# Performance work log

Measured on AMD Instinct MI355X. Metric: run time of the kernel, lower is better.

The kernel has to match this reference:

```python
import jax, jax.numpy as jnp
import numpy as np

B, T, S = 32, 64, 64
V, E, H, Hs = 32000, 512, 512, 512
D2 = 2 * Hs  # src feature dim


def setup_inputs() -> dict:
    key = jax.random.key(0)
    ks = jax.random.split(key, 26)
    n = lambda k, shape, s=0.05: (jax.random.normal(k, shape, jnp.float32) * s)
    inp = {
        'src': jax.random.normal(ks[0], (B, S, D2), jnp.float32),
        'trg': jax.random.randint(ks[1], (B, T), 0, V),
        'mask': jnp.ones((B, T), jnp.float32),
        'emb': n(ks[2], (V, E)),
        # PyTorch LSTMCell params: weight_ih [4H, E+H], weight_hh [4H, H]
        'f_Wih': n(ks[3], (4 * H, E + H)), 'f_Whh': n(ks[4], (4 * H, H)),
        'f_bih': n(ks[5], (4 * H,)), 'f_bhh': n(ks[6], (4 * H,)),
        'b_Wih': n(ks[7], (4 * H, E + H)), 'b_Whh': n(ks[8], (4 * H, H)),
        'b_bih': n(ks[9], (4 * H,)), 'b_bhh': n(ks[10], (4 * H,)),
        # attention projections: hidden -> 2*src_hidden
        'fatt_W': n(ks[11], (D2, H)), 'fatt_b': n(ks[12], (D2,)),
        'batt_W': n(ks[13], (D2, H)), 'batt_b': n(ks[14], (D2,)),
        # att_hidden linears: (H + 2*Hs) -> H
        'fah_W': n(ks[15], (H, H + D2)), 'fah_b': n(ks[16], (H,)),
        'bah_W': n(ks[17], (H, H + D2)), 'bah_b': n(ks[18], (H,)),
        # output projection 2H -> V
        'fc_W': n(ks[19], (V, 2 * H)), 'fc_b': n(ks[20], (V,)),
        'feed_init': n(ks[21], (2 * H,), 1.0),
        'hid_init': n(ks[22], (4 * H,), 1.0),
    }
    return inp


def reference(src, trg, mask, emb, f_Wih, f_Whh, f_bih, f_bhh,
              b_Wih, b_Whh, b_bih, b_bhh, fatt_W, fatt_b, batt_W, batt_b,
              fah_W, fah_b, bah_W, bah_b, fc_W, fc_b, feed_init, hid_init):
    Bn = src.shape[0]
    Hn = feed_init.shape[0] // 2
    scale = 1.0 / np.sqrt(Hn)  # key.size(-1) == trg hidden before projection

    x = emb[trg]  # [B, T, E]  (dropout p=0 -> identity)

    hhat0 = jnp.broadcast_to(feed_init, (Bn, 2 * Hn))
    f_hhat0, b_hhat0 = jnp.split(hhat0, 2, axis=1)
    hid0 = jnp.broadcast_to(hid_init, (Bn, 4 * Hn))
    f_hid, b_hid = jnp.split(hid0, 2, axis=-1)
    f_h0, f_c0 = jnp.split(f_hid, 2, axis=-1)
    b_h0, b_c0 = jnp.split(b_hid, 2, axis=-1)

    def lstm(xin, h, c, Wih, Whh, bih, bhh):
        g = xin @ Wih.T + bih + h @ Whh.T + bhh
        i, f, gg, o = jnp.split(g, 4, axis=-1)
        c = jax.nn.sigmoid(f) * c + jax.nn.sigmoid(i) * jnp.tanh(gg)
        h = jax.nn.sigmoid(o) * jnp.tanh(c)
        return h, c

    def att(h, W, b):
        k = h @ W.T + b                              # [B, 2Hs]
        w = jnp.einsum('bd,bsd->bs', k, src) * scale  # [B, S]
        p = jax.nn.softmax(w, axis=-1)
        return jnp.einsum('bs,bsd->bd', p, src)       # [B, 2Hs]

    xs = jnp.swapaxes(x, 0, 1)      # [T, B, E]
    ms = jnp.swapaxes(mask, 0, 1)   # [T, B]

    def f_step(carry, x_t):
        h, c, hhat = carry
        h, c = lstm(jnp.concatenate([x_t, hhat], -1), h, c, f_Wih, f_Whh, f_bih, f_bhh)
        ct = att(h, fatt_W, fatt_b)
        # NOTE: original uses b_att_hidden in the forward loop (faithful)
        hhat = jnp.tanh(jnp.concatenate([h, ct], -1) @ bah_W.T + bah_b)
        return (h, c, hhat), hhat

    _, f_out = jax.lax.scan(f_step, (f_h0, f_c0, f_hhat0), xs)  # [T, B, H]

    def b_step(carry, inp):
        x_t, m_t = inp
        h, c, hhat = carry
        hn, cn = lstm(jnp.concatenate([x_t, hhat], -1), h, c, b_Wih, b_Whh, b_bih, b_bhh)
        h = m_t[:, None] * hn
        c = m_t[:, None] * cn
        ct = att(h, batt_W, batt_b)
        # NOTE: original uses f_att_hidden in the backward loop (faithful)
        hhat = jnp.tanh(jnp.concatenate([h, ct], -1) @ fah_W.T + fah_b)
        return (h, c, hhat), hhat

    _, b_out = jax.lax.scan(b_step, (b_h0, b_c0, b_hhat0), (xs[::-1], ms[::-1]))

    f_out = jnp.swapaxes(f_out, 0, 1)        # [B, T, H]
    b_cheat = jnp.swapaxes(b_out, 0, 1)      # reversed-time order, as stacked in torch
    # b_outputs[:, :-2] = b_outputs_cheat[:, 2:]; last two steps zero (faithful)
    b_shift = jnp.concatenate([b_cheat[:, 2:], jnp.zeros_like(b_cheat[:, :2])], axis=1)

    logits = jnp.concatenate([f_out, b_shift], -1) @ fc_W.T + fc_b  # [B, T, V]
    return logits
```

## Files before the change

### kernel.cpp

```cpp
#include <hip/hip_runtime.h>
#include <hip/hip_bf16.h>
#include <math.h>

typedef __hip_bfloat16 bf16;
typedef __attribute__((ext_vector_type(8))) short short8b;
typedef __attribute__((ext_vector_type(8))) __bf16 bf16x8;
typedef __attribute__((ext_vector_type(4))) float f32x4;

#define SCALE_F 0.04419417382415922f

template <typename V>
static __device__ inline auto mfma_try(V a, V b, f32x4 c, int)
    -> decltype(__builtin_amdgcn_mfma_f32_16x16x32_bf16(a, b, c, 0, 0, 0)) {
  return __builtin_amdgcn_mfma_f32_16x16x32_bf16(a, b, c, 0, 0, 0);
}
template <typename V>
static __device__ inline auto mfma_try(V a, V b, f32x4 c, long)
    -> decltype(__builtin_amdgcn_mfma_f32_16x16x32_bf16(
        __builtin_bit_cast(bf16x8, a), __builtin_bit_cast(bf16x8, b), c, 0, 0, 0)) {
  return __builtin_amdgcn_mfma_f32_16x16x32_bf16(
      __builtin_bit_cast(bf16x8, a), __builtin_bit_cast(bf16x8, b), c, 0, 0, 0);
}
static __device__ inline f32x4 MFMA(short8b a, short8b b, f32x4 c) {
  return mfma_try(a, b, c, 0);
}

static __device__ inline short8b ldb8(const bf16* p) {
  return *reinterpret_cast<const short8b*>(p);
}
static __device__ inline float b2f(bf16 v) { return __bfloat162float(v); }
static __device__ inline bf16 f2b(float v) { return __float2bfloat16(v); }
static __device__ inline float s2f(short s) {
  unsigned u = ((unsigned)(unsigned short)s) << 16;
  return __builtin_bit_cast(float, u);
}
static __device__ inline unsigned pack2(float lo, float hi) {
  const unsigned a = (unsigned)__builtin_bit_cast(unsigned short, f2b(lo));
  const unsigned b = (unsigned)__builtin_bit_cast(unsigned short, f2b(hi));
  return a | (b << 16);
}
static __device__ inline float sigm(float x) { return 1.f / (1.f + expf(-x)); }

static __device__ inline void st2_wt(bf16* p, float v) {
  unsigned ud = (unsigned)__builtin_bit_cast(unsigned short, f2b(v));
  asm volatile("global_store_short %0, %1, off sc0 sc1" ::"v"(p), "v"(ud)
               : "memory");
}
static __device__ inline void st4_wt(bf16* p, float lo, float hi) {
  unsigned ud = pack2(lo, hi);
  asm volatile("global_store_dword %0, %1, off sc0 sc1" ::"v"(p), "v"(ud)
               : "memory");
}

static __device__ inline void st_flag(unsigned* p, unsigned v) {
  asm volatile("global_store_dword %0, %1, off sc0 sc1" ::"v"(p), "v"(v)
               : "memory");
}
static __device__ inline unsigned ld_flag(const unsigned* p) {
  unsigned v;
  asm volatile("global_load_dword %0, %1, off sc0 sc1\n\ts_waitcnt vmcnt(0)"
               : "=v"(v)
               : "v"(p)
               : "memory");
  return v;
}

static __device__ inline void gbar(unsigned* flags, unsigned ep, int blk, int tid) {
  asm volatile("s_waitcnt vmcnt(0)" ::: "memory");
  __syncthreads();
  if (tid < 64) {
    unsigned* row = flags + (size_t)ep * 64;
    if (tid == 0) st_flag(row + blk, 1u);
    while (true) {
      const unsigned v = ld_flag(row + tid);
      if (__ballot(v != 0) == ~0ull) break;
      __builtin_amdgcn_s_sleep(1);
    }
  }
  __syncthreads();
}

template <typename OutT, bool HAS_BIAS>
__global__ __launch_bounds__(256) void gemm_k(
    const bf16* __restrict__ A, const bf16* __restrict__ Bw,
    OutT* __restrict__ C, const float* __restrict__ bias,
    int M, int N, int K) {
  const int lane = threadIdx.x & 63;
  const int wid = threadIdx.x >> 6;
  const int m0 = blockIdx.y * 128 + (wid >> 1) * 64;
  const int n0 = blockIdx.x * 128 + (wid & 1) * 64;
  const int lr = lane & 15;
  const int lk = (lane >> 4) * 8;
  f32x4 acc[4][4];
#pragma unroll
  for (int i = 0; i < 4; ++i)
#pragma unroll
    for (int j = 0; j < 4; ++j) acc[i][j] = (f32x4){0.f, 0.f, 0.f, 0.f};
  const bf16* Ap = A + (size_t)(m0 + lr) * K + lk;
  const bf16* Bp = Bw + (size_t)(n0 + lr) * K + lk;
  for (int k0 = 0; k0 < K; k0 += 32) {
    short8b av[4], bv[4];
#pragma unroll
    for (int i = 0; i < 4; ++i) av[i] = ldb8(Ap + (size_t)i * 16 * K + k0);
#pragma unroll
    for (int i = 0; i < 4; ++i) bv[i] = ldb8(Bp + (size_t)i * 16 * K + k0);
#pragma unroll
    for (int mi = 0; mi < 4; ++mi)
#pragma unroll
      for (int ni = 0; ni < 4; ++ni)
        acc[mi][ni] = MFMA(av[mi], bv[ni], acc[mi][ni]);
  }
  const int rb = (lane >> 4) * 4;
#pragma unroll
  for (int mi = 0; mi < 4; ++mi) {
#pragma unroll
    for (int r = 0; r < 4; ++r) {
      const int row = m0 + mi * 16 + rb + r;
#pragma unroll
      for (int ni = 0; ni < 4; ++ni) {
        const int col = n0 + ni * 16 + lr;
        float v = acc[mi][ni][r];
        if (HAS_BIAS) v += bias[col];
        if constexpr (sizeof(OutT) == 2) {
          C[(size_t)row * N + col] = f2b(v);
        } else {
          C[(size_t)row * N + col] = v;
        }
      }
    }
  }
}

__global__ void k_xg(const float* __restrict__ emb, const int* __restrict__ trg,
                     bf16* __restrict__ xg) {
  const int i = blockIdx.x * 256 + threadIdx.x;
  const int r = i >> 9, e = i & 511;
  const int t = r >> 5, b = r & 31;
  const int tok = trg[b * 64 + t];
  xg[i] = f2b(emb[(size_t)tok * 512 + e]);
}

__global__ void k_srcb(const float* __restrict__ s, bf16* __restrict__ d) {
  const int i = blockIdx.x * 256 + threadIdx.x;
  d[i] = f2b(s[i]);
}

__global__ void k_fcw(const float* __restrict__ s, bf16* __restrict__ d) {
  const size_t stride = (size_t)gridDim.x * blockDim.x;
  for (size_t i = blockIdx.x * (size_t)blockDim.x + threadIdx.x;
       i < (size_t)32000 * 1024; i += stride)
    d[i] = f2b(s[i]);
}

__global__ void k_bmt(const bf16* __restrict__ in, bf16* __restrict__ out) {
  const int i = blockIdx.x * 256 + threadIdx.x;
  const int b = i >> 15, rem = i & 32767, o = rem >> 6, s = rem & 63;
  out[i] = in[(size_t)(b * 64 + s) * 512 + o];
}

__global__ void k_wpack(const float* __restrict__ fWih, const float* __restrict__ fWhh,
                        const float* __restrict__ bWih, const float* __restrict__ bWhh,
                        const float* __restrict__ fattW, const float* __restrict__ battW,
                        const float* __restrict__ bahW, const float* __restrict__ fahW,
                        bf16* Wxf, bf16* Wxb, bf16* Wrecf, bf16* Wrecb,
                        bf16* attWtf, bf16* attWtb, bf16* ahW2f, bf16* ahW2b,
                        bf16* Wh1f, bf16* Wh1b) {
  const int stride = gridDim.x * blockDim.x;
  const int i0 = blockIdx.x * blockDim.x + threadIdx.x;
  for (int i = i0; i < 2048 * 512; i += stride) {
    const int gc = i >> 9, k = i & 511;
    Wxf[i] = f2b(fWih[(size_t)gc * 1024 + k]);
    Wxb[i] = f2b(bWih[(size_t)gc * 1024 + k]);
  }
  for (int i = i0; i < 2048 * 1024; i += stride) {
    const int gc = i >> 10, k = i & 1023;
    float vf, vb;
    if (k < 512) { vf = fWih[(size_t)gc * 1024 + 512 + k]; vb = bWih[(size_t)gc * 1024 + 512 + k]; }
    else         { vf = fWhh[(size_t)gc * 512 + k - 512]; vb = bWhh[(size_t)gc * 512 + k - 512]; }
    Wrecf[i] = f2b(vf); Wrecb[i] = f2b(vb);
  }
  for (int i = i0; i < 512 * 1024; i += stride) {
    const int j = i >> 10, d = i & 1023;
    attWtf[i] = f2b(fattW[(size_t)d * 512 + j]);
    attWtb[i] = f2b(battW[(size_t)d * 512 + j]);
  }
  for (int i = i0; i < 512 * 1024; i += stride) {
    const int o = i >> 10, d = i & 1023;
    ahW2f[i] = f2b(bahW[(size_t)o * 1536 + 512 + d]);
    ahW2b[i] = f2b(fahW[(size_t)o * 1536 + 512 + d]);
  }
  for (int i = i0; i < 512 * 512; i += stride) {
    const int o = i >> 9, k = i & 511;
    Wh1f[i] = f2b(bahW[(size_t)o * 1536 + k]);
    Wh1b[i] = f2b(fahW[(size_t)o * 1536 + k]);
  }
}

__global__ void k_c0(const float* __restrict__ src, const float* __restrict__ fb,
                     const float* __restrict__ bb, float* __restrict__ c0f,
                     float* __restrict__ c0b) {
  const int r = blockIdx.x;
  const int tid = threadIdx.x;
  float pf = 0.f, pb = 0.f;
  for (int d = tid; d < 1024; d += 256) {
    const float s = src[(size_t)r * 1024 + d];
    pf += s * fb[d];
    pb += s * bb[d];
  }
#pragma unroll
  for (int d = 1; d < 64; d <<= 1) { pf += __shfl_xor(pf, d); pb += __shfl_xor(pb, d); }
  __shared__ float rf[4], rb2[4];
  if ((tid & 63) == 0) { rf[tid >> 6] = pf; rb2[tid >> 6] = pb; }
  __syncthreads();
  if (tid == 0) {
    c0f[r] = (rf[0] + rf[1] + rf[2] + rf[3]) * SCALE_F;
    c0b[r] = (rb2[0] + rb2[1] + rb2[2] + rb2[3]) * SCALE_F;
  }
}

__global__ void k_init(const float* __restrict__ feed, const float* __restrict__ hid,
                       bf16* hh0, bf16* hh1, bf16* hb0, bf16* hb1,
                       float* cst0, float* cst1) {
  const int i = blockIdx.x * 256 + threadIdx.x;
  const int b = i >> 9, k = i & 511;
  hh0[i] = f2b(feed[k]);
  hh1[i] = f2b(feed[512 + k]);
  hb0[i] = f2b(hid[k]);
  hb1[i] = f2b(hid[1024 + k]);
  cst0[k * 32 + b] = hid[512 + k];
  cst1[k * 32 + b] = hid[1536 + k];
}

struct ScanP {
  const bf16* Wrec[2]; const bf16* Xp[2]; const bf16* Af[2]; const bf16* Bmt[2];
  const bf16* Wh1[2]; const float* bih[2]; const float* bhh[2];
  const float* c0[2]; const float* ahb[2]; const float* mask;
  bf16* hh[2]; bf16* hb[2]; bf16* U[2]; float* cst[2]; bf16* hcat; unsigned* flags;
};

__global__ __launch_bounds__(256) void scan_k(ScanP P) {
  const int blk = blockIdx.x;
  const int dir = blk >> 5;
  const int g = blk & 31;
  const int tid = threadIdx.x;
  const int lane = tid & 63;
  const int wv = tid >> 6;

  const bf16* __restrict__ Wrec = P.Wrec[dir];
  const bf16* __restrict__ Xp = P.Xp[dir];
  const bf16* __restrict__ Af = P.Af[dir];
  const bf16* __restrict__ Bmt = P.Bmt[dir];
  const bf16* __restrict__ Wh1 = P.Wh1[dir];
  const float* __restrict__ bihp = P.bih[dir];
  const float* __restrict__ bhhp = P.bhh[dir];
  const float* __restrict__ c0v = P.c0[dir];
  const float* __restrict__ ahbp = P.ahb[dir];
  bf16* __restrict__ hhB = P.hh[dir];
  bf16* __restrict__ hbB = P.hb[dir];
  bf16* __restrict__ Ubuf = P.U[dir];
  float* __restrict__ cst = P.cst[dir];

  __shared__ float gl[4][16][33];
  __shared__ float h_lds[512];
  __shared__ float w_part[2][64];
  __shared__ float p_lds[64];

  unsigned ep = 0;
  const int lr16 = lane & 15;
  const int kb = lane >> 4;
  const int koff = kb * 8;

  short8b pA0[16], pA1[16];
  {
    const bf16* A0 = hbB + (size_t)lr16 * 512;
    const bf16* A1 = hbB + (size_t)(lr16 + 16) * 512;
#pragma unroll
    for (int ks = 0; ks < 16; ++ks) {
      pA0[ks] = ldb8(A0 + ks * 32 + koff);
      pA1[ks] = ldb8(A1 + ks * 32 + koff);
    }
  }

  for (int t = 0; t < 64; ++t) {
    const bf16* hhR = hhB + (size_t)t * 32 * 512;
    bf16* hhW = hhB + (size_t)(t + 1) * 32 * 512;
    bf16* hbW = hbB + (size_t)(t + 1) * 32 * 512;

    {
      const int gate = wv;
      const int gc = gate * 512 + g * 16 + lr16;
      const bf16* Brow = Wrec + (size_t)gc * 1024;
      const bf16* A0h = hhR + (size_t)lr16 * 512;
      const bf16* A1h = hhR + (size_t)(lr16 + 16) * 512;
      f32x4 ac0 = (f32x4){0.f, 0.f, 0.f, 0.f};
      f32x4 ac1 = (f32x4){0.f, 0.f, 0.f, 0.f};
#pragma unroll
      for (int ks = 0; ks < 16; ++ks) {
        const int k = ks * 32 + koff;
        const short8b bv = ldb8(Brow + 512 + k);
        ac0 = MFMA(pA0[ks], bv, ac0);
        ac1 = MFMA(pA1[ks], bv, ac1);
      }
#pragma unroll
      for (int c = 0; c < 2; ++c) {
        short8b sa[8], sb[8];
#pragma unroll
        for (int i = 0; i < 8; ++i) {
          const int k = (c * 8 + i) * 32 + koff;
          sa[i] = ldb8(A0h + k);
          sb[i] = ldb8(A1h + k);
        }
#pragma unroll
        for (int i = 0; i < 8; ++i) {
          const int k = (c * 8 + i) * 32 + koff;
          const short8b bv = ldb8(Brow + k);
          ac0 = MFMA(sa[i], bv, ac0);
          ac1 = MFMA(sb[i], bv, ac1);
        }
      }
      const int tcol = dir ? (63 - t) : t;
      const float bsum = bihp[gc] + bhhp[gc];
      const bf16* xpc = Xp + (size_t)gc * 2048 + tcol * 32;
#pragma unroll
      for (int r = 0; r < 4; ++r) {
        const int brow = kb * 4 + r;
        gl[gate][lr16][brow] = ac0[r] + b2f(xpc[brow]) + bsum;
        gl[gate][lr16][brow + 16] = ac1[r] + b2f(xpc[brow + 16]) + bsum;
      }
    }
    __syncthreads();
    {
      const int b = tid & 31;
      const int jp = (tid >> 5) * 2;
      float hn2[2];
#pragma unroll
      for (int u = 0; u < 2; ++u) {
        const int jl = jp + u;
        const int j = g * 16 + jl;
        const float gi = gl[0][jl][b];
        const float gf = gl[1][jl][b];
        const float gg = gl[2][jl][b];
        const float go = gl[3][jl][b];
        float cn = sigm(gf) * cst[j * 32 + b] + sigm(gi) * tanhf(gg);
        float hn = sigm(go) * tanhf(cn);
        if (dir) {
          const float m = P.mask[b * 64 + (63 - t)];
          hn *= m; cn *= m;
        }
        cst[j * 32 + b] = cn;
        hn2[u] = hn;
      }
      st4_wt(hbW + (size_t)b * 512 + g * 16 + jp, hn2[0], hn2[1]);
    }
    gbar(P.flags, ep++, blk, tid);

    if (wv == 0) {
      const bf16* Brow = Wh1 + (size_t)(g * 16 + lr16) * 512;
      const bf16* A0 = hbW + (size_t)lr16 * 512;
      const bf16* A1 = hbW + (size_t)(lr16 + 16) * 512;
      f32x4 u0 = (f32x4){0.f, 0.f, 0.f, 0.f};
      f32x4 u1 = (f32x4){0.f, 0.f, 0.f, 0.f};
#pragma unroll
      for (int ks = 0; ks < 16; ++ks) {
        const int k = ks * 32 + koff;
        const short8b bv = ldb8(Brow + k);
        u0 = MFMA(ldb8(A0 + k), bv, u0);
        u1 = MFMA(ldb8(A1 + k), bv, u1);
      }
      bf16* Uw = Ubuf + (size_t)t * 32 * 512;
      const int o = g * 16 + lr16;
#pragma unroll
      for (int r = 0; r < 4; ++r) {
        const int b0 = kb * 4 + r;
        st2_wt(Uw + (size_t)b0 * 512 + o, u0[r]);
        st2_wt(Uw + (size_t)(b0 + 16) * 512 + o, u1[r]);
      }
    } else if (wv == 1) {
      const short8b v = ldb8(hbW + (size_t)g * 512 + lane * 8);
#pragma unroll
      for (int e = 0; e < 8; ++e) h_lds[lane * 8 + e] = s2f(v[e]);
    }
    __syncthreads();
    if (wv == 1 || wv == 2) {
      const int q = wv - 1;
      const bf16* arow = Af + (size_t)(g * 64 + lane) * 512 + q * 256;
      float part = 0.f;
#pragma unroll 8
      for (int k8 = 0; k8 < 256; k8 += 8) {
        const short8b v = ldb8(arow + k8);
#pragma unroll
        for (int e = 0; e < 8; ++e) part += h_lds[q * 256 + k8 + e] * s2f(v[e]);
      }
      w_part[q][lane] = part;
    }
    __syncthreads();
    if (wv == 3) {
      const float v = (w_part[0][lane] + w_part[1][lane]) * SCALE_F + c0v[g * 64 + lane];
      float mx = v;
#pragma unroll
      for (int d = 1; d < 64; d <<= 1) mx = fmaxf(mx, __shfl_xor(mx, d));
      const float e = expf(v - mx);
      float sm = e;
#pragma unroll
      for (int d = 1; d < 64; d <<= 1) sm += __shfl_xor(sm, d);
      p_lds[lane] = e / sm;
    }
    __syncthreads();
    float a2[2];
    {
      const int o2 = tid * 2;
      const bf16* bm0 = Bmt + ((size_t)g * 512 + o2) * 64;
      short8b v0[8], v1[8];
#pragma unroll
      for (int i = 0; i < 8; ++i) {
        v0[i] = ldb8(bm0 + i * 8);
        v1[i] = ldb8(bm0 + 64 + i * 8);
      }
      float s0 = ahbp[o2], s1 = ahbp[o2 + 1];
#pragma unroll
      for (int i = 0; i < 8; ++i)
#pragma unroll
        for (int e = 0; e < 8; ++e) {
          const float p = p_lds[i * 8 + e];
          s0 += p * s2f(v0[i][e]);
          s1 += p * s2f(v1[i][e]);
        }
      a2[0] = s0; a2[1] = s1;
    }
    gbar(P.flags, ep++, blk, tid);

    {
      const int o2 = tid * 2;
      const unsigned uu =
          *reinterpret_cast<const unsigned*>(Ubuf + ((size_t)t * 32 + g) * 512 + o2);
      const float h0 = tanhf(a2[0] + s2f((short)(uu & 0xffffu)));
      const float h1 = tanhf(a2[1] + s2f((short)(uu >> 16)));
      st4_wt(hhW + (size_t)g * 512 + o2, h0, h1);
      const unsigned hp = pack2(h0, h1);
      if (dir == 0) {
        *reinterpret_cast<unsigned*>(P.hcat + (size_t)(g * 64 + t) * 1024 + o2) = hp;
      } else if (t >= 2) {
        *reinterpret_cast<unsigned*>(P.hcat + (size_t)(g * 64 + t - 2) * 1024 + 512 + o2) = hp;
      }
      if (t < 63) {
        const bf16* A0 = hbW + (size_t)lr16 * 512;
        const bf16* A1 = hbW + (size_t)(lr16 + 16) * 512;
#pragma unroll
        for (int ks = 0; ks < 16; ++ks) {
          pA0[ks] = ldb8(A0 + ks * 32 + koff);
          pA1[ks] = ldb8(A1 + ks * 32 + koff);
        }
      }
    }
    gbar(P.flags, ep++, blk, tid);
  }
}

extern "C" void kernel_launch(void* const* d_in, const int* in_sizes, int n_in,
                              void* d_out, int out_size, void* d_ws, size_t ws_size,
                              hipStream_t stream) {
  (void)in_sizes; (void)n_in; (void)out_size; (void)ws_size;
  const float* src  = (const float*)d_in[0];
  const int*   trg  = (const int*)d_in[1];
  const float* mask = (const float*)d_in[2];
  const float* emb  = (const float*)d_in[3];
  const float* fWih = (const float*)d_in[4];
  const float* fWhh = (const float*)d_in[5];
  const float* fbih = (const float*)d_in[6];
  const float* fbhh = (const float*)d_in[7];
  const float* bWih = (const float*)d_in[8];
  const float* bWhh = (const float*)d_in[9];
  const float* bbih = (const float*)d_in[10];
  const float* bbhh = (const float*)d_in[11];
  const float* fattW = (const float*)d_in[12];
  const float* fattb = (const float*)d_in[13];
  const float* battW = (const float*)d_in[14];
  const float* battb = (const float*)d_in[15];
  const float* fahW = (const float*)d_in[16];
  const float* fahb = (const float*)d_in[17];
  const float* bahW = (const float*)d_in[18];
  const float* bahb = (const float*)d_in[19];
  const float* fcW  = (const float*)d_in[20];
  const float* fcb  = (const float*)d_in[21];
  const float* feed = (const float*)d_in[22];
  const float* hid  = (const float*)d_in[23];

  char* wsp = (char*)d_ws;
  size_t off = 0;
  auto alloc = [&](size_t bytes) -> void* {
    void* p = wsp + off;
    off += (bytes + 255) & ~(size_t)255;
    return p;
  };
  unsigned* flags = (unsigned*)alloc((size_t)192 * 64 * 4);
  bf16* hcat = (bf16*)alloc((size_t)2048 * 1024 * 2);
  const size_t zero_bytes = off;
  bf16* xg    = (bf16*)alloc((size_t)2048 * 512 * 2);
  bf16* srcb  = (bf16*)alloc((size_t)2048 * 1024 * 2);
  bf16* fcWb  = (bf16*)alloc((size_t)32000 * 1024 * 2);
  bf16* Wxf   = (bf16*)alloc((size_t)2048 * 512 * 2);
  bf16* Wxb   = (bf16*)alloc((size_t)2048 * 512 * 2);
  bf16* Wrecf = (bf16*)alloc((size_t)2048 * 1024 * 2);
  bf16* Wrecb = (bf16*)alloc((size_t)2048 * 1024 * 2);
  bf16* attWtf = (bf16*)alloc((size_t)512 * 1024 * 2);
  bf16* attWtb = (bf16*)alloc((size_t)512 * 1024 * 2);
  bf16* ahW2f = (bf16*)alloc((size_t)512 * 1024 * 2);
  bf16* ahW2b = (bf16*)alloc((size_t)512 * 1024 * 2);
  bf16* Wh1f  = (bf16*)alloc((size_t)512 * 512 * 2);
  bf16* Wh1b  = (bf16*)alloc((size_t)512 * 512 * 2);
  bf16* Xpf   = (bf16*)alloc((size_t)2048 * 2048 * 2);
  bf16* Xpb   = (bf16*)alloc((size_t)2048 * 2048 * 2);
  bf16* Aff   = (bf16*)alloc((size_t)2048 * 512 * 2);
  bf16* Afb   = (bf16*)alloc((size_t)2048 * 512 * 2);
  bf16* Bmf   = (bf16*)alloc((size_t)2048 * 512 * 2);
  bf16* Bmb   = (bf16*)alloc((size_t)2048 * 512 * 2);
  bf16* Bmtf  = (bf16*)alloc((size_t)2048 * 512 * 2);
  bf16* Bmtb  = (bf16*)alloc((size_t)2048 * 512 * 2);
  float* c0f  = (float*)alloc(2048 * 4);
  float* c0b  = (float*)alloc(2048 * 4);
  bf16* hh0   = (bf16*)alloc((size_t)65 * 32 * 512 * 2);
  bf16* hh1   = (bf16*)alloc((size_t)65 * 32 * 512 * 2);
  bf16* hb0   = (bf16*)alloc((size_t)65 * 32 * 512 * 2);
  bf16* hb1   = (bf16*)alloc((size_t)65 * 32 * 512 * 2);
  bf16* Uf    = (bf16*)alloc((size_t)64 * 32 * 512 * 2);
  bf16* Ub    = (bf16*)alloc((size_t)64 * 32 * 512 * 2);
  float* cst0 = (float*)alloc((size_t)512 * 32 * 4);
  float* cst1 = (float*)alloc((size_t)512 * 32 * 4);

  hipMemsetAsync(d_ws, 0, zero_bytes, stream);

  k_xg<<<4096, 256, 0, stream>>>(emb, trg, xg);
  k_srcb<<<8192, 256, 0, stream>>>(src, srcb);
  k_fcw<<<8192, 256, 0, stream>>>(fcW, fcWb);
  k_wpack<<<2048, 256, 0, stream>>>(fWih, fWhh, bWih, bWhh, fattW, battW, bahW, fahW,
                                    Wxf, Wxb, Wrecf, Wrecb, attWtf, attWtb, ahW2f, ahW2b,
                                    Wh1f, Wh1b);
  k_c0<<<2048, 256, 0, stream>>>(src, fattb, battb, c0f, c0b);
  k_init<<<64, 256, 0, stream>>>(feed, hid, hh0, hh1, hb0, hb1, cst0, cst1);

  gemm_k<bf16, false><<<dim3(16, 16), 256, 0, stream>>>(Wxf, xg, Xpf, nullptr, 2048, 2048, 512);
  gemm_k<bf16, false><<<dim3(16, 16), 256, 0, stream>>>(Wxb, xg, Xpb, nullptr, 2048, 2048, 512);
  gemm_k<bf16, false><<<dim3(4, 16), 256, 0, stream>>>(srcb, attWtf, Aff, nullptr, 2048, 512, 1024);
  gemm_k<bf16, false><<<dim3(4, 16), 256, 0, stream>>>(srcb, attWtb, Afb, nullptr, 2048, 512, 1024);
  gemm_k<bf16, false><<<dim3(4, 16), 256, 0, stream>>>(srcb, ahW2f, Bmf, nullptr, 2048, 512, 1024);
  gemm_k<bf16, false><<<dim3(4, 16), 256, 0, stream>>>(srcb, ahW2b, Bmb, nullptr, 2048, 512, 1024);
  k_bmt<<<4096, 256, 0, stream>>>(Bmf, Bmtf);
  k_bmt<<<4096, 256, 0, stream>>>(Bmb, Bmtb);

  ScanP sp;
  sp.Wrec[0] = Wrecf; sp.Wrec[1] = Wrecb;
  sp.Xp[0] = Xpf;     sp.Xp[1] = Xpb;
  sp.Af[0] = Aff;     sp.Af[1] = Afb;
  sp.Bmt[0] = Bmtf;   sp.Bmt[1] = Bmtb;
  sp.Wh1[0] = Wh1f;   sp.Wh1[1] = Wh1b;
  sp.bih[0] = fbih;   sp.bih[1] = bbih;
  sp.bhh[0] = fbhh;   sp.bhh[1] = bbhh;
  sp.c0[0] = c0f;     sp.c0[1] = c0b;
  sp.ahb[0] = bahb;   sp.ahb[1] = fahb;
  sp.mask = mask;
  sp.hh[0] = hh0;     sp.hh[1] = hh1;
  sp.hb[0] = hb0;     sp.hb[1] = hb1;
  sp.U[0] = Uf;       sp.U[1] = Ub;
  sp.cst[0] = cst0;   sp.cst[1] = cst1;
  sp.hcat = hcat;     sp.flags = flags;
  scan_k<<<64, 256, 0, stream>>>(sp);

  gemm_k<float, true><<<dim3(250, 16), 256, 0, stream>>>(hcat, fcWb, (float*)d_out, fcb,
                                                         2048, 32000, 1024);
}
```

Baseline: 2.867 ms.

## Replace persistent scan kernel with per-timestep kernel launches

The single persistent scan kernel, which used flag-based global barriers three times per step, is replaced by two kernel launches per timestep (LSTM gates, then attention plus att_hidden). The Wh1 projection is folded into the second kernel as a per-thread dot product, which removes the intermediate U buffer and one barrier. Stream ordering now supplies grid-wide synchronisation, at the cost of 128 kernel launches and no cross-step register reuse of the hb operands.

```diff
diff --git a/kernel.cpp b/kernel.cpp
--- a/kernel.cpp
+++ b/kernel.cpp
@@ -40,45 +40,6 @@
   return a | (b << 16);
 }
 static __device__ inline float sigm(float x) { return 1.f / (1.f + expf(-x)); }
-
-static __device__ inline void st2_wt(bf16* p, float v) {
-  unsigned ud = (unsigned)__builtin_bit_cast(unsigned short, f2b(v));
-  asm volatile("global_store_short %0, %1, off sc0 sc1" ::"v"(p), "v"(ud)
-               : "memory");
-}
-static __device__ inline void st4_wt(bf16* p, float lo, float hi) {
-  unsigned ud = pack2(lo, hi);
-  asm volatile("global_store_dword %0, %1, off sc0 sc1" ::"v"(p), "v"(ud)
-               : "memory");
-}
-
-static __device__ inline void st_flag(unsigned* p, unsigned v) {
-  asm volatile("global_store_dword %0, %1, off sc0 sc1" ::"v"(p), "v"(v)
-               : "memory");
-}
-static __device__ inline unsigned ld_flag(const unsigned* p) {
-  unsigned v;
-  asm volatile("global_load_dword %0, %1, off sc0 sc1\n\ts_waitcnt vmcnt(0)"
-               : "=v"(v)
-               : "v"(p)
-               : "memory");
-  return v;
-}
-
-static __device__ inline void gbar(unsigned* flags, unsigned ep, int blk, int tid) {
-  asm volatile("s_waitcnt vmcnt(0)" ::: "memory");
-  __syncthreads();
-  if (tid < 64) {
-    unsigned* row = flags + (size_t)ep * 64;
-    if (tid == 0) st_flag(row + blk, 1u);
-    while (true) {
-      const unsigned v = ld_flag(row + tid);
-      if (__ballot(v != 0) == ~0ull) break;
-      __builtin_amdgcn_s_sleep(1);
-    }
-  }
-  __syncthreads();
-}
 
 template <typename OutT, bool HAS_BIAS>
 __global__ __launch_bounds__(256) void gemm_k(
@@ -231,14 +192,14 @@
   cst1[k * 32 + b] = hid[1536 + k];
 }
 
-struct ScanP {
+struct StepP {
   const bf16* Wrec[2]; const bf16* Xp[2]; const bf16* Af[2]; const bf16* Bmt[2];
   const bf16* Wh1[2]; const float* bih[2]; const float* bhh[2];
   const float* c0[2]; const float* ahb[2]; const float* mask;
-  bf16* hh[2]; bf16* hb[2]; bf16* U[2]; float* cst[2]; bf16* hcat; unsigned* flags;
+  bf16* hh[2]; bf16* hb[2]; float* cst[2]; bf16* hcat;
 };
 
-__global__ __launch_bounds__(256) void scan_k(ScanP P) {
+__global__ __launch_bounds__(256) void k_step_a(StepP P, int t) {
   const int blk = blockIdx.x;
   const int dir = blk >> 5;
   const int g = blk & 31;
@@ -248,211 +209,197 @@
 
   const bf16* __restrict__ Wrec = P.Wrec[dir];
   const bf16* __restrict__ Xp = P.Xp[dir];
+  const float* __restrict__ bihp = P.bih[dir];
+  const float* __restrict__ bhhp = P.bhh[dir];
+  float* __restrict__ cst = P.cst[dir];
+
+  const bf16* hhR = P.hh[dir] + (size_t)t * 32 * 512;
+  const bf16* hbR = P.hb[dir] + (size_t)t * 32 * 512;
+  bf16* hbW = P.hb[dir] + (size_t)(t + 1) * 32 * 512;
+
+  __shared__ float gl[4][16][33];
+  const int lr16 = lane & 15;
+  const int kb = lane >> 4;
+  const int koff = kb * 8;
+
+  {
+    const int gate = wv;
+    const int gc = gate * 512 + g * 16 + lr16;
+    const bf16* Brow = Wrec + (size_t)gc * 1024;
+    const bf16* A0h = hhR + (size_t)lr16 * 512;
+    const bf16* A1h = hhR + (size_t)(lr16 + 16) * 512;
+    const bf16* A0g = hbR + (size_t)lr16 * 512;
+    const bf16* A1g = hbR + (size_t)(lr16 + 16) * 512;
+    f32x4 ac0 = (f32x4){0.f, 0.f, 0.f, 0.f};
+    f32x4 ac1 = (f32x4){0.f, 0.f, 0.f, 0.f};
+#pragma unroll
+    for (int c = 0; c < 2; ++c) {
+      short8b sa[8], sb[8];
+#pragma unroll
+      for (int i = 0; i < 8; ++i) {
+        const int k = (c * 8 + i) * 32 + koff;
+        sa[i] = ldb8(A0g + k);
+        sb[i] = ldb8(A1g + k);
+      }
+#pragma unroll
+      for (int i = 0; i < 8; ++i) {
+        const int k = (c * 8 + i) * 32 + koff;
+        const short8b bv = ldb8(Brow + 512 + k);
+        ac0 = MFMA(sa[i], bv, ac0);
+        ac1 = MFMA(sb[i], bv, ac1);
+      }
+    }
+#pragma unroll
+    for (int c = 0; c < 2; ++c) {
+      short8b sa[8], sb[8];
+#pragma unroll
+      for (int i = 0; i < 8; ++i) {
+        const int k = (c * 8 + i) * 32 + koff;
+        sa[i] = ldb8(A0h + k);
+        sb[i] = ldb8(A1h + k);
+      }
+#pragma unroll
+      for (int i = 0; i < 8; ++i) {
+        const int k = (c * 8 + i) * 32 + koff;
+        const short8b bv = ldb8(Brow + k);
+        ac0 = MFMA(sa[i], bv, ac0);
+        ac1 = MFMA(sb[i], bv, ac1);
+      }
+    }
+    const int tcol = dir ? (63 - t) : t;
+    const float bsum = bihp[gc] + bhhp[gc];
+    const bf16* xpc = Xp + (size_t)gc * 2048 + tcol * 32;
+#pragma unroll
+    for (int r = 0; r < 4; ++r) {
+      const int brow = kb * 4 + r;
+      gl[gate][lr16][brow] = ac0[r] + b2f(xpc[brow]) + bsum;
+      gl[gate][lr16][brow + 16] = ac1[r] + b2f(xpc[brow + 16]) + bsum;
+    }
+  }
+  __syncthreads();
+  {
+    const int b = tid & 31;
+    const int jp = (tid >> 5) * 2;
+    float hn2[2];
+#pragma unroll
+    for (int u = 0; u < 2; ++u) {
+      const int jl = jp + u;
+      const int j = g * 16 + jl;
+      const float gi = gl[0][jl][b];
+      const float gf = gl[1][jl][b];
+      const float gg = gl[2][jl][b];
+      const float go = gl[3][jl][b];
+      float cn = sigm(gf) * cst[j * 32 + b] + sigm(gi) * tanhf(gg);
+      float hn = sigm(go) * tanhf(cn);
+      if (dir) {
+        const float m = P.mask[b * 64 + (63 - t)];
+        hn *= m; cn *= m;
+      }
+      cst[j * 32 + b] = cn;
+      hn2[u] = hn;
+    }
+    *reinterpret_cast<unsigned*>(hbW + (size_t)b * 512 + g * 16 + jp) =
+        pack2(hn2[0], hn2[1]);
+  }
+}
+
+__global__ __launch_bounds__(256) void k_step_b(StepP P, int t) {
+  const int blk = blockIdx.x;
+  const int dir = blk >> 5;
+  const int g = blk & 31;
+  const int tid = threadIdx.x;
+  const int lane = tid & 63;
+  const int wv = tid >> 6;
+
   const bf16* __restrict__ Af = P.Af[dir];
   const bf16* __restrict__ Bmt = P.Bmt[dir];
   const bf16* __restrict__ Wh1 = P.Wh1[dir];
-  const float* __restrict__ bihp = P.bih[dir];
-  const float* __restrict__ bhhp = P.bhh[dir];
   const float* __restrict__ c0v = P.c0[dir];
   const float* __restrict__ ahbp = P.ahb[dir];
-  bf16* __restrict__ hhB = P.hh[dir];
-  bf16* __restrict__ hbB = P.hb[dir];
-  bf16* __restrict__ Ubuf = P.U[dir];
-  float* __restrict__ cst = P.cst[dir];
-
-  __shared__ float gl[4][16][33];
+
+  const bf16* hbW = P.hb[dir] + (size_t)(t + 1) * 32 * 512;
+  bf16* hhW = P.hh[dir] + (size_t)(t + 1) * 32 * 512;
+
   __shared__ float h_lds[512];
-  __shared__ float w_part[2][64];
+  __shared__ float w_part[4][64];
   __shared__ float p_lds[64];
 
-  unsigned ep = 0;
-  const int lr16 = lane & 15;
-  const int kb = lane >> 4;
-  const int koff = kb * 8;
-
-  short8b pA0[16], pA1[16];
+  if (tid < 64) {
+    const short8b v = ldb8(hbW + (size_t)g * 512 + tid * 8);
+#pragma unroll
+    for (int e = 0; e < 8; ++e) h_lds[tid * 8 + e] = s2f(v[e]);
+  }
+  __syncthreads();
   {
-    const bf16* A0 = hbB + (size_t)lr16 * 512;
-    const bf16* A1 = hbB + (size_t)(lr16 + 16) * 512;
-#pragma unroll
-    for (int ks = 0; ks < 16; ++ks) {
-      pA0[ks] = ldb8(A0 + ks * 32 + koff);
-      pA1[ks] = ldb8(A1 + ks * 32 + koff);
-    }
-  }
-
-  for (int t = 0; t < 64; ++t) {
-    const bf16* hhR = hhB + (size_t)t * 32 * 512;
-    bf16* hhW = hhB + (size_t)(t + 1) * 32 * 512;
-    bf16* hbW = hbB + (size_t)(t + 1) * 32 * 512;
-
-    {
-      const int gate = wv;
-      const int gc = gate * 512 + g * 16 + lr16;
-      const bf16* Brow = Wrec + (size_t)gc * 1024;
-      const bf16* A0h = hhR + (size_t)lr16 * 512;
-      const bf16* A1h = hhR + (size_t)(lr16 + 16) * 512;
-      f32x4 ac0 = (f32x4){0.f, 0.f, 0.f, 0.f};
-      f32x4 ac1 = (f32x4){0.f, 0.f, 0.f, 0.f};
-#pragma unroll
-      for (int ks = 0; ks < 16; ++ks) {
-        const int k = ks * 32 + koff;
-        const short8b bv = ldb8(Brow + 512 + k);
-        ac0 = MFMA(pA0[ks], bv, ac0);
-        ac1 = MFMA(pA1[ks], bv, ac1);
-      }
-#pragma unroll
-      for (int c = 0; c < 2; ++c) {
-        short8b sa[8], sb[8];
-#pragma unroll
-        for (int i = 0; i < 8; ++i) {
-          const int k = (c * 8 + i) * 32 + koff;
-          sa[i] = ldb8(A0h + k);
-          sb[i] = ldb8(A1h + k);
-        }
-#pragma unroll
-        for (int i = 0; i < 8; ++i) {
-          const int k = (c * 8 + i) * 32 + koff;
-          const short8b bv = ldb8(Brow + k);
-          ac0 = MFMA(sa[i], bv, ac0);
-          ac1 = MFMA(sb[i], bv, ac1);
-        }
-      }
-      const int tcol = dir ? (63 - t) : t;
-      const float bsum = bihp[gc] + bhhp[gc];
-      const bf16* xpc = Xp + (size_t)gc * 2048 + tcol * 32;
-#pragma unroll
-      for (int r = 0; r < 4; ++r) {
-        const int brow = kb * 4 + r;
-        gl[gate][lr16][brow] = ac0[r] + b2f(xpc[brow]) + bsum;
-        gl[gate][lr16][brow + 16] = ac1[r] + b2f(xpc[brow + 16]) + bsum;
-      }
-    }
-    __syncthreads();
-    {
-      const int b = tid & 31;
-      const int jp = (tid >> 5) * 2;
-      float hn2[2];
-#pragma unroll
-      for (int u = 0; u < 2; ++u) {
-        const int jl = jp + u;
-        const int j = g * 16 + jl;
-        const float gi = gl[0][jl][b];
-        const float gf = gl[1][jl][b];
-        const float gg = gl[2][jl][b];
-        const float go = gl[3][jl][b];
-        float cn = sigm(gf) * cst[j * 32 + b] + sigm(gi) * tanhf(gg);
-        float hn = sigm(go) * tanhf(cn);
-        if (dir) {
-          const float m = P.mask[b * 64 + (63 - t)];
-          hn *= m; cn *= m;
-        }
-        cst[j * 32 + b] = cn;
-        hn2[u] = hn;
-      }
-      st4_wt(hbW + (size_t)b * 512 + g * 16 + jp, hn2[0], hn2[1]);
-    }
-    gbar(P.flags, ep++, blk, tid);
-
-    if (wv == 0) {
-      const bf16* Brow = Wh1 + (size_t)(g * 16 + lr16) * 512;
-      const bf16* A0 = hbW + (size_t)lr16 * 512;
-      const bf16* A1 = hbW + (size_t)(lr16 + 16) * 512;
-      f32x4 u0 = (f32x4){0.f, 0.f, 0.f, 0.f};
-      f32x4 u1 = (f32x4){0.f, 0.f, 0.f, 0.f};
-#pragma unroll
-      for (int ks = 0; ks < 16; ++ks) {
-        const int k = ks * 32 + koff;
-        const short8b bv = ldb8(Brow + k);
-        u0 = MFMA(ldb8(A0 + k), bv, u0);
-        u1 = MFMA(ldb8(A1 + k), bv, u1);
-      }
-      bf16* Uw = Ubuf + (size_t)t * 32 * 512;
-      const int o = g * 16 + lr16;
-#pragma unroll
-      for (int r = 0; r < 4; ++r) {
-        const int b0 = kb * 4 + r;
-        st2_wt(Uw + (size_t)b0 * 512 + o, u0[r]);
-        st2_wt(Uw + (size_t)(b0 + 16) * 512 + o, u1[r]);
-      }
-    } else if (wv == 1) {
-      const short8b v = ldb8(hbW + (size_t)g * 512 + lane * 8);
-#pragma unroll
-      for (int e = 0; e < 8; ++e) h_lds[lane * 8 + e] = s2f(v[e]);
-    }
-    __syncthreads();
-    if (wv == 1 || wv == 2) {
-      const int q = wv - 1;
-      const bf16* arow = Af + (size_t)(g * 64 + lane) * 512 + q * 256;
-      float part = 0.f;
+    const int q = wv;
+    const bf16* arow = Af + (size_t)(g * 64 + lane) * 512 + q * 128;
+    float part = 0.f;
 #pragma unroll 8
-      for (int k8 = 0; k8 < 256; k8 += 8) {
-        const short8b v = ldb8(arow + k8);
-#pragma unroll
-        for (int e = 0; e < 8; ++e) part += h_lds[q * 256 + k8 + e] * s2f(v[e]);
-      }
-      w_part[q][lane] = part;
-    }
-    __syncthreads();
-    if (wv == 3) {
-      const float v = (w_part[0][lane] + w_part[1][lane]) * SCALE_F + c0v[g * 64 + lane];
-      float mx = v;
-#pragma unroll
-      for (int d = 1; d < 64; d <<= 1) mx = fmaxf(mx, __shfl_xor(mx, d));
-      const float e = expf(v - mx);
-      float sm = e;
-#pragma unroll
-      for (int d = 1; d < 64; d <<= 1) sm += __shfl_xor(sm, d);
-      p_lds[lane] = e / sm;
-    }
-    __syncthreads();
-    float a2[2];
-    {
-      const int o2 = tid * 2;
-      const bf16* bm0 = Bmt + ((size_t)g * 512 + o2) * 64;
-      short8b v0[8], v1[8];
-#pragma unroll
-      for (int i = 0; i < 8; ++i) {
-        v0[i] = ldb8(bm0 + i * 8);
-        v1[i] = ldb8(bm0 + 64 + i * 8);
-      }
-      float s0 = ahbp[o2], s1 = ahbp[o2 + 1];
-#pragma unroll
-      for (int i = 0; i < 8; ++i)
-#pragma unroll
-        for (int e = 0; e < 8; ++e) {
-          const float p = p_lds[i * 8 + e];
-          s0 += p * s2f(v0[i][e]);
-          s1 += p * s2f(v1[i][e]);
-        }
-      a2[0] = s0; a2[1] = s1;
-    }
-    gbar(P.flags, ep++, blk, tid);
-
-    {
-      const int o2 = tid * 2;
-      const unsigned uu =
-          *reinterpret_cast<const unsigned*>(Ubuf + ((size_t)t * 32 + g) * 512 + o2);
-      const float h0 = tanhf(a2[0] + s2f((short)(uu & 0xffffu)));
-      const float h1 = tanhf(a2[1] + s2f((short)(uu >> 16)));
-      st4_wt(hhW + (size_t)g * 512 + o2, h0, h1);
-      const unsigned hp = pack2(h0, h1);
-      if (dir == 0) {
-        *reinterpret_cast<unsigned*>(P.hcat + (size_t)(g * 64 + t) * 1024 + o2) = hp;
-      } else if (t >= 2) {
-        *reinterpret_cast<unsigned*>(P.hcat + (size_t)(g * 64 + t - 2) * 1024 + 512 + o2) = hp;
-      }
-      if (t < 63) {
-        const bf16* A0 = hbW + (size_t)lr16 * 512;
-        const bf16* A1 = hbW + (size_t)(lr16 + 16) * 512;
-#pragma unroll
-        for (int ks = 0; ks < 16; ++ks) {
-          pA0[ks] = ldb8(A0 + ks * 32 + koff);
-          pA1[ks] = ldb8(A1 + ks * 32 + koff);
-        }
-      }
-    }
-    gbar(P.flags, ep++, blk, tid);
+    for (int k8 = 0; k8 < 128; k8 += 8) {
+      const short8b v = ldb8(arow + k8);
+#pragma unroll
+      for (int e = 0; e < 8; ++e) part += h_lds[q * 128 + k8 + e] * s2f(v[e]);
+    }
+    w_part[q][lane] = part;
+  }
+  __syncthreads();
+  if (wv == 3) {
+    const float v = (w_part[0][lane] + w_part[1][lane] + w_part[2][lane] +
+                     w_part[3][lane]) * SCALE_F + c0v[g * 64 + lane];
+    float mx = v;
+#pragma unroll
+    for (int d = 1; d < 64; d <<= 1) mx = fmaxf(mx, __shfl_xor(mx, d));
+    const float e = expf(v - mx);
+    float sm = e;
+#pragma unroll
+    for (int d = 1; d < 64; d <<= 1) sm += __shfl_xor(sm, d);
+    p_lds[lane] = e / sm;
+  }
+  __syncthreads();
+
+  const int o2 = tid * 2;
+  float u0 = 0.f, u1 = 0.f;
+  {
+    const bf16* w0 = Wh1 + (size_t)o2 * 512;
+    const bf16* w1 = w0 + 512;
+#pragma unroll 4
+    for (int k8 = 0; k8 < 512; k8 += 8) {
+      const short8b wa = ldb8(w0 + k8);
+      const short8b wb = ldb8(w1 + k8);
+#pragma unroll
+      for (int e = 0; e < 8; ++e) {
+        const float hv = h_lds[k8 + e];
+        u0 += hv * s2f(wa[e]);
+        u1 += hv * s2f(wb[e]);
+      }
+    }
+  }
+  float s0 = ahbp[o2], s1 = ahbp[o2 + 1];
+  {
+    const bf16* bm0 = Bmt + ((size_t)g * 512 + o2) * 64;
+    short8b v0[8], v1[8];
+#pragma unroll
+    for (int i = 0; i < 8; ++i) {
+      v0[i] = ldb8(bm0 + i * 8);
+      v1[i] = ldb8(bm0 + 64 + i * 8);
+    }
+#pragma unroll
+    for (int i = 0; i < 8; ++i)
+#pragma unroll
+      for (int e = 0; e < 8; ++e) {
+        const float p = p_lds[i * 8 + e];
+        s0 += p * s2f(v0[i][e]);
+        s1 += p * s2f(v1[i][e]);
+      }
+  }
+  const float h0 = tanhf(u0 + s0);
+  const float h1 = tanhf(u1 + s1);
+  *reinterpret_cast<unsigned*>(hhW + (size_t)g * 512 + o2) = pack2(h0, h1);
+  const unsigned hp = pack2(h0, h1);
+  if (dir == 0) {
+    *reinterpret_cast<unsigned*>(P.hcat + (size_t)(g * 64 + t) * 1024 + o2) = hp;
+  } else if (t >= 2) {
+    *reinterpret_cast<unsigned*>(P.hcat + (size_t)(g * 64 + t - 2) * 1024 + 512 + o2) = hp;
   }
 }
 
@@ -492,7 +439,6 @@
     off += (bytes + 255) & ~(size_t)255;
     return p;
   };
-  unsigned* flags = (unsigned*)alloc((size_t)192 * 64 * 4);
   bf16* hcat = (bf16*)alloc((size_t)2048 * 1024 * 2);
   const size_t zero_bytes = off;
   bf16* xg    = (bf16*)alloc((size_t)2048 * 512 * 2);
@@ -522,8 +468,6 @@
   bf16* hh1   = (bf16*)alloc((size_t)65 * 32 * 512 * 2);
   bf16* hb0   = (bf16*)alloc((size_t)65 * 32 * 512 * 2);
   bf16* hb1   = (bf16*)alloc((size_t)65 * 32 * 512 * 2);
-  bf16* Uf    = (bf16*)alloc((size_t)64 * 32 * 512 * 2);
-  bf16* Ub    = (bf16*)alloc((size_t)64 * 32 * 512 * 2);
   float* cst0 = (float*)alloc((size_t)512 * 32 * 4);
   float* cst1 = (float*)alloc((size_t)512 * 32 * 4);
 
@@ -547,7 +491,7 @@
   k_bmt<<<4096, 256, 0, stream>>>(Bmf, Bmtf);
   k_bmt<<<4096, 256, 0, stream>>>(Bmb, Bmtb);
 
-  ScanP sp;
+  StepP sp;
   sp.Wrec[0] = Wrecf; sp.Wrec[1] = Wrecb;
   sp.Xp[0] = Xpf;     sp.Xp[1] = Xpb;
   sp.Af[0] = Aff;     sp.Af[1] = Afb;
@@ -560,10 +504,13 @@
   sp.mask = mask;
   sp.hh[0] = hh0;     sp.hh[1] = hh1;
   sp.hb[0] = hb0;     sp.hb[1] = hb1;
-  sp.U[0] = Uf;       sp.U[1] = Ub;
   sp.cst[0] = cst0;   sp.cst[1] = cst1;
-  sp.hcat = hcat;     sp.flags = flags;
-  scan_k<<<64, 256, 0, stream>>>(sp);
+  sp.hcat = hcat;
+
+  for (int t = 0; t < 64; ++t) {
+    k_step_a<<<64, 256, 0, stream>>>(sp, t);
+    k_step_b<<<64, 256, 0, stream>>>(sp, t);
+  }
 
   gemm_k<float, true><<<dim3(250, 16), 256, 0, stream>>>(hcat, fcWb, (float*)d_out, fcb,
                                                          2048, 32000, 1024);
```

Result: slower. 3.058 ms (+6.7%).

## Drop a grid barrier by computing the Wh1 projection locally, remap output GEMM tiles across XCDs

Applied to the files above, without the earlier changes.

In the recurrent scan, each block used to compute a slice of the h@Wh1 projection with MFMA, write it to a global U buffer, and wait on an extra grid-wide barrier before reading back its own batch row. Now each block computes the full 512-wide projection for its own batch row from LDS with scalar FMAs, which removes one grid barrier per timestep and the U buffer round-trip. The cost is redundant per-block work and streaming all of Wh1 through each block every step. The attention score dot product is also split across all four waves instead of two. Separately, the final vocabulary GEMM becomes a dedicated kernel that maps a 1D grid to tiles so that each XCD gets a contiguous run of tiles, aiming for better L2 reuse.

```diff
diff --git a/kernel.cpp b/kernel.cpp
--- a/kernel.cpp
+++ b/kernel.cpp
@@ -41,11 +41,6 @@
 }
 static __device__ inline float sigm(float x) { return 1.f / (1.f + expf(-x)); }
 
-static __device__ inline void st2_wt(bf16* p, float v) {
-  unsigned ud = (unsigned)__builtin_bit_cast(unsigned short, f2b(v));
-  asm volatile("global_store_short %0, %1, off sc0 sc1" ::"v"(p), "v"(ud)
-               : "memory");
-}
 static __device__ inline void st4_wt(bf16* p, float lo, float hi) {
   unsigned ud = pack2(lo, hi);
   asm volatile("global_store_dword %0, %1, off sc0 sc1" ::"v"(p), "v"(ud)
@@ -126,6 +121,54 @@
         } else {
           C[(size_t)row * N + col] = v;
         }
+      }
+    }
+  }
+}
+
+__global__ __launch_bounds__(256) void gemm_out(
+    const bf16* __restrict__ A, const bf16* __restrict__ Bw,
+    float* __restrict__ C, const float* __restrict__ bias) {
+  const int K = 1024, N = 32000;
+  const int wgid = blockIdx.x;
+  const int xcd = wgid & 7, loc = wgid >> 3;
+  const int T = xcd * 500 + loc;
+  const int mt = T & 15, nt = T >> 4;
+  const int lane = threadIdx.x & 63;
+  const int wid = threadIdx.x >> 6;
+  const int m0 = mt * 128 + (wid >> 1) * 64;
+  const int n0 = nt * 128 + (wid & 1) * 64;
+  const int lr = lane & 15;
+  const int lk = (lane >> 4) * 8;
+  f32x4 acc[4][4];
+#pragma unroll
+  for (int i = 0; i < 4; ++i)
+#pragma unroll
+    for (int j = 0; j < 4; ++j) acc[i][j] = (f32x4){0.f, 0.f, 0.f, 0.f};
+  const bf16* Ap = A + (size_t)(m0 + lr) * K + lk;
+  const bf16* Bp = Bw + (size_t)(n0 + lr) * K + lk;
+  for (int k0 = 0; k0 < K; k0 += 32) {
+    short8b av[4], bv[4];
+#pragma unroll
+    for (int i = 0; i < 4; ++i) av[i] = ldb8(Ap + (size_t)i * 16 * K + k0);
+#pragma unroll
+    for (int i = 0; i < 4; ++i) bv[i] = ldb8(Bp + (size_t)i * 16 * K + k0);
+#pragma unroll
+    for (int mi = 0; mi < 4; ++mi)
+#pragma unroll
+      for (int ni = 0; ni < 4; ++ni)
+        acc[mi][ni] = MFMA(av[mi], bv[ni], acc[mi][ni]);
+  }
+  const int rb = (lane >> 4) * 4;
+#pragma unroll
+  for (int mi = 0; mi < 4; ++mi) {
+#pragma unroll
+    for (int r = 0; r < 4; ++r) {
+      const int row = m0 + mi * 16 + rb + r;
+#pragma unroll
+      for (int ni = 0; ni < 4; ++ni) {
+        const int col = n0 + ni * 16 + lr;
+        C[(size_t)row * N + col] = acc[mi][ni][r] + bias[col];
       }
     }
   }
@@ -235,7 +278,7 @@
   const bf16* Wrec[2]; const bf16* Xp[2]; const bf16* Af[2]; const bf16* Bmt[2];
   const bf16* Wh1[2]; const float* bih[2]; const float* bhh[2];
   const float* c0[2]; const float* ahb[2]; const float* mask;
-  bf16* hh[2]; bf16* hb[2]; bf16* U[2]; float* cst[2]; bf16* hcat; unsigned* flags;
+  bf16* hh[2]; bf16* hb[2]; float* cst[2]; bf16* hcat; unsigned* flags;
 };
 
 __global__ __launch_bounds__(256) void scan_k(ScanP P) {
@@ -257,12 +300,11 @@
   const float* __restrict__ ahbp = P.ahb[dir];
   bf16* __restrict__ hhB = P.hh[dir];
   bf16* __restrict__ hbB = P.hb[dir];
-  bf16* __restrict__ Ubuf = P.U[dir];
   float* __restrict__ cst = P.cst[dir];
 
   __shared__ float gl[4][16][33];
   __shared__ float h_lds[512];
-  __shared__ float w_part[2][64];
+  __shared__ float w_part[4][64];
   __shared__ float p_lds[64];
 
   unsigned ep = 0;
@@ -354,48 +396,28 @@
     }
     gbar(P.flags, ep++, blk, tid);
 
-    if (wv == 0) {
-      const bf16* Brow = Wh1 + (size_t)(g * 16 + lr16) * 512;
-      const bf16* A0 = hbW + (size_t)lr16 * 512;
-      const bf16* A1 = hbW + (size_t)(lr16 + 16) * 512;
-      f32x4 u0 = (f32x4){0.f, 0.f, 0.f, 0.f};
-      f32x4 u1 = (f32x4){0.f, 0.f, 0.f, 0.f};
-#pragma unroll
-      for (int ks = 0; ks < 16; ++ks) {
-        const int k = ks * 32 + koff;
-        const short8b bv = ldb8(Brow + k);
-        u0 = MFMA(ldb8(A0 + k), bv, u0);
-        u1 = MFMA(ldb8(A1 + k), bv, u1);
-      }
-      bf16* Uw = Ubuf + (size_t)t * 32 * 512;
-      const int o = g * 16 + lr16;
-#pragma unroll
-      for (int r = 0; r < 4; ++r) {
-        const int b0 = kb * 4 + r;
-        st2_wt(Uw + (size_t)b0 * 512 + o, u0[r]);
-        st2_wt(Uw + (size_t)(b0 + 16) * 512 + o, u1[r]);
-      }
-    } else if (wv == 1) {
-      const short8b v = ldb8(hbW + (size_t)g * 512 + lane * 8);
-#pragma unroll
-      for (int e = 0; e < 8; ++e) h_lds[lane * 8 + e] = s2f(v[e]);
+    if (tid < 64) {
+      const short8b v = ldb8(hbW + (size_t)g * 512 + tid * 8);
+#pragma unroll
+      for (int e = 0; e < 8; ++e) h_lds[tid * 8 + e] = s2f(v[e]);
     }
     __syncthreads();
-    if (wv == 1 || wv == 2) {
-      const int q = wv - 1;
-      const bf16* arow = Af + (size_t)(g * 64 + lane) * 512 + q * 256;
+    {
+      const int q = wv;
+      const bf16* arow = Af + (size_t)(g * 64 + lane) * 512 + q * 128;
       float part = 0.f;
 #pragma unroll 8
-      for (int k8 = 0; k8 < 256; k8 += 8) {
+      for (int k8 = 0; k8 < 128; k8 += 8) {
         const short8b v = ldb8(arow + k8);
 #pragma unroll
-        for (int e = 0; e < 8; ++e) part += h_lds[q * 256 + k8 + e] * s2f(v[e]);
+        for (int e = 0; e < 8; ++e) part += h_lds[q * 128 + k8 + e] * s2f(v[e]);
       }
       w_part[q][lane] = part;
     }
     __syncthreads();
     if (wv == 3) {
-      const float v = (w_part[0][lane] + w_part[1][lane]) * SCALE_F + c0v[g * 64 + lane];
+      const float v = (w_part[0][lane] + w_part[1][lane] + w_part[2][lane] +
+                       w_part[3][lane]) * SCALE_F + c0v[g * 64 + lane];
       float mx = v;
 #pragma unroll
       for (int d = 1; d < 64; d <<= 1) mx = fmaxf(mx, __shfl_xor(mx, d));
@@ -406,35 +428,44 @@
       p_lds[lane] = e / sm;
     }
     __syncthreads();
-    float a2[2];
     {
       const int o2 = tid * 2;
-      const bf16* bm0 = Bmt + ((size_t)g * 512 + o2) * 64;
-      short8b v0[8], v1[8];
-#pragma unroll
-      for (int i = 0; i < 8; ++i) {
-        v0[i] = ldb8(bm0 + i * 8);
-        v1[i] = ldb8(bm0 + 64 + i * 8);
+      float u0 = 0.f, u1 = 0.f;
+      {
+        const bf16* w0 = Wh1 + (size_t)o2 * 512;
+        const bf16* w1 = w0 + 512;
+#pragma unroll 4
+        for (int k8 = 0; k8 < 512; k8 += 8) {
+          const short8b wa = ldb8(w0 + k8);
+          const short8b wb = ldb8(w1 + k8);
+#pragma unroll
+          for (int e = 0; e < 8; ++e) {
+            const float hv = h_lds[k8 + e];
+            u0 += hv * s2f(wa[e]);
+            u1 += hv * s2f(wb[e]);
+          }
+        }
       }
       float s0 = ahbp[o2], s1 = ahbp[o2 + 1];
-#pragma unroll
-      for (int i = 0; i < 8; ++i)
-#pragma unroll
-        for (int e = 0; e < 8; ++e) {
-          const float p = p_lds[i * 8 + e];
-          s0 += p * s2f(v0[i][e]);
-          s1 += p * s2f(v1[i][e]);
-        }
-      a2[0] = s0; a2[1] = s1;
-    }
-    gbar(P.flags, ep++, blk, tid);
-
-    {
-      const int o2 = tid * 2;
-      const unsigned uu =
-          *reinterpret_cast<const unsigned*>(Ubuf + ((size_t)t * 32 + g) * 512 + o2);
-      const float h0 = tanhf(a2[0] + s2f((short)(uu & 0xffffu)));
-      const float h1 = tanhf(a2[1] + s2f((short)(uu >> 16)));
+      {
+        const bf16* bm0 = Bmt + ((size_t)g * 512 + o2) * 64;
+        short8b v0[8], v1[8];
+#pragma unroll
+        for (int i = 0; i < 8; ++i) {
+          v0[i] = ldb8(bm0 + i * 8);
+          v1[i] = ldb8(bm0 + 64 + i * 8);
+        }
+#pragma unroll
+        for (int i = 0; i < 8; ++i)
+#pragma unroll
+          for (int e = 0; e < 8; ++e) {
+            const float p = p_lds[i * 8 + e];
+            s0 += p * s2f(v0[i][e]);
+            s1 += p * s2f(v1[i][e]);
+          }
+      }
+      const float h0 = tanhf(u0 + s0);
+      const float h1 = tanhf(u1 + s1);
       st4_wt(hhW + (size_t)g * 512 + o2, h0, h1);
       const unsigned hp = pack2(h0, h1);
       if (dir == 0) {
@@ -522,8 +553,6 @@
   bf16* hh1   = (bf16*)alloc((size_t)65 * 32 * 512 * 2);
   bf16* hb0   = (bf16*)alloc((size_t)65 * 32 * 512 * 2);
   bf16* hb1   = (bf16*)alloc((size_t)65 * 32 * 512 * 2);
-  bf16* Uf    = (bf16*)alloc((size_t)64 * 32 * 512 * 2);
-  bf16* Ub    = (bf16*)alloc((size_t)64 * 32 * 512 * 2);
   float* cst0 = (float*)alloc((size_t)512 * 32 * 4);
   float* cst1 = (float*)alloc((size_t)512 * 32 * 4);
 
@@ -560,11 +589,9 @@
   sp.mask = mask;
   sp.hh[0] = hh0;     sp.hh[1] = hh1;
   sp.hb[0] = hb0;     sp.hb[1] = hb1;
-  sp.U[0] = Uf;       sp.U[1] = Ub;
   sp.cst[0] = cst0;   sp.cst[1] = cst1;
   sp.hcat = hcat;     sp.flags = flags;
   scan_k<<<64, 256, 0, stream>>>(sp);
 
-  gemm_k<float, true><<<dim3(250, 16), 256, 0, stream>>>(hcat, fcWb, (float*)d_out, fcb,
-                                                         2048, 32000, 1024);
-}
+  gemm_out<<<4000, 256, 0, stream>>>(hcat, fcWb, (float*)d_out, fcb);
+}
```

New measurement: 3.382 ms. 18.0% more time.
